# Performance work log

Hardware: AMD Instinct MI355X
Metric: run time of the kernel (lower is better)

The kernel has to match this reference:

```python
import jax, jax.numpy as jnp
import numpy as np

# ---- Cl(3,0) Cayley table derivation (pure Python, done once at import) ----
_BASIS_GENS = [(), (1,), (2,), (3,), (1, 2), (1, 3), (2, 3), (1, 2, 3)]
_GENS_TO_IDX = {g: i for i, g in enumerate(_BASIS_GENS)}

def _reduce_product(a_gens, b_gens):
    gens = list(a_gens) + list(b_gens)
    sign = 1
    changed = True
    while changed:
        changed = False
        i = 0
        while i < len(gens) - 1:
            if gens[i] == gens[i + 1]:
                gens.pop(i); gens.pop(i)
                changed = True
                if i > 0:
                    i -= 1
            elif gens[i] > gens[i + 1]:
                gens[i], gens[i + 1] = gens[i + 1], gens[i]
                sign *= -1
                changed = True
                i += 1
            else:
                i += 1
    return _GENS_TO_IDX[tuple(gens)], sign

def _k_groups():
    gi = [[] for _ in range(8)]
    gj = [[] for _ in range(8)]
    gs = [[] for _ in range(8)]
    for i in range(8):
        for j in range(8):
            k, s = _reduce_product(_BASIS_GENS[i], _BASIS_GENS[j])
            gi[k].append(i); gj[k].append(j); gs[k].append(float(s))
    return np.array(gi), np.array(gj), np.array(gs, dtype=np.float32)

KG_I, KG_J, KG_S = _k_groups()  # each (8, 8): for target blade k, 8 (i,j,sign) contributions
LN_EPS = 1e-5


def setup_inputs() -> dict:
    key = jax.random.key(0)
    ks = jax.random.split(key, 6)
    B, T, N, D, Fdim = 4, 4096, 8, 128, 512
    return {
        "x": jax.random.normal(ks[0], (B, T, N, D), dtype=jnp.float32),
        "interaction_weights": 0.1 * jax.random.normal(ks[1], (N, N), dtype=jnp.float32),
        "w_gate": 0.02 * jax.random.normal(ks[2], (D, Fdim), dtype=jnp.float32),
        "w_up": 0.02 * jax.random.normal(ks[3], (D, Fdim), dtype=jnp.float32),
        "w_down": 0.02 * jax.random.normal(ks[4], (Fdim, D), dtype=jnp.float32),
        "ln_gamma": jnp.ones((D,), dtype=jnp.float32),
        "ln_beta": jnp.zeros((D,), dtype=jnp.float32),
        "geo_gate": jnp.float32(0.5),
    }


def reference(x, interaction_weights, w_gate, w_up, w_down, ln_gamma, ln_beta, geo_gate):
    # x: (B, T, 8, D)
    kg_i = jnp.asarray(KG_I)
    kg_j = jnp.asarray(KG_J)
    kg_s = jnp.asarray(KG_S)

    # K-grouped Cayley geometric self-product
    w = jax.nn.sigmoid(interaction_weights)          # (8, 8)
    sw = kg_s * w[kg_i, kg_j]                        # (8, 8): sign * weight per (k, pair)
    x_i = x[:, :, kg_i, :]                           # (B, T, 8, 8, D)
    x_j = x[:, :, kg_j, :]                           # (B, T, 8, 8, D)
    geo = jnp.sum(x_i * x_j * sw[None, None, :, :, None], axis=3)  # (B, T, 8, D)

    # gate-mix geo with residual stream
    gate = jax.nn.sigmoid(geo_gate)
    mixed = gate * geo + (1.0 - gate) * x

    # LayerNorm over last dim
    mu = jnp.mean(mixed, axis=-1, keepdims=True)
    var = jnp.var(mixed, axis=-1, keepdims=True)
    normed = (mixed - mu) / jnp.sqrt(var + LN_EPS) * ln_gamma + ln_beta

    # per-blade SwiGLU FFN
    g = normed @ w_gate                              # (B, T, 8, F)
    u = normed @ w_up
    out = (jax.nn.silu(g) * u) @ w_down              # (B, T, 8, D)
    return x + out
```

## Files before the change

### kernel.cpp

```cpp
#include <hip/hip_runtime.h>


typedef __bf16 bf16x8 __attribute__((ext_vector_type(8)));
typedef float  f32x4  __attribute__((ext_vector_type(4)));

#define MFMA16(a, b, c) __builtin_amdgcn_mfma_f32_16x16x32_bf16((a), (b), (c), 0, 0, 0)

constexpr int OFF_WG = 0;
constexpr int OFF_WU = 131072;
constexpr int OFF_WD = 262144;
constexpr int OFF_C  = 393216;

__device__ __forceinline__ float fexp2(float x) {
  float r; asm("v_exp_f32 %0, %1" : "=v"(r) : "v"(x)); return r;
}
__device__ __forceinline__ float frcp(float x) {
  float r; asm("v_rcp_f32 %0, %1" : "=v"(r) : "v"(x)); return r;
}
__device__ __forceinline__ float fsigmoid(float x) {
  return frcp(1.f + fexp2(-1.44269504088896f * x));
}
__device__ __forceinline__ unsigned cvtbf(float f) {
  unsigned u = __builtin_bit_cast(unsigned, f);
  return (u + 0x7fffu + ((u >> 16) & 1u)) >> 16;
}
__device__ __forceinline__ unsigned pack2(float a, float b) {
  return cvtbf(a) | (cvtbf(b) << 16);
}

__device__ constexpr int PIdx[7][4][2] = {
  {{0,1},{2,4},{3,5},{6,7}},
  {{0,2},{1,4},{3,6},{5,7}},
  {{0,3},{1,5},{2,6},{4,7}},
  {{0,4},{1,2},{3,7},{5,6}},
  {{0,5},{1,3},{2,7},{4,6}},
  {{0,6},{1,7},{2,3},{4,5}},
  {{0,7},{1,6},{2,5},{3,4}}};

__global__ __launch_bounds__(256) void k_prep(
    const float* __restrict__ W, const float* __restrict__ wg,
    const float* __restrict__ wu, const float* __restrict__ wd,
    const float* __restrict__ gg, char* __restrict__ ws) {
  int gid = blockIdx.x * 256 + threadIdx.x;
  if (gid < 65536) {
    int f = gid & 511, k = gid >> 9;
    unsigned short v = (unsigned short)cvtbf(wg[k * 512 + f]);
    int fl = f & 63;
    int off = OFF_WG + (f >> 6) * 16384 + ((fl * 256 + k * 2) ^ ((f & 7) << 4));
    *(unsigned short*)(ws + off) = v;
  } else if (gid < 131072) {
    int t = gid - 65536;
    int f = t & 511, k = t >> 9;
    unsigned short v = (unsigned short)cvtbf(wu[k * 512 + f]);
    int fl = f & 63;
    int off = OFF_WU + (f >> 6) * 16384 + ((fl * 256 + k * 2) ^ ((f & 7) << 4));
    *(unsigned short*)(ws + off) = v;
  } else {
    int t = gid - 131072;
    int d = t & 127, f = t >> 7;
    unsigned short v = (unsigned short)cvtbf(wd[f * 128 + d]);
    int fl = f & 63;
    int off = OFF_WD + (f >> 6) * 16384 + ((d * 128 + fl * 2) ^ ((d & 7) << 4));
    *(unsigned short*)(ws + off) = v;
  }
  if (blockIdx.x == 0 && threadIdx.x == 0) {
    float s[64];
    for (int i = 0; i < 64; ++i) s[i] = fsigmoid(W[i]);
    float* C = (float*)(ws + OFF_C);
#define Sij(i, j) s[(i) * 8 + (j)]
    for (int i = 0; i < 8; ++i) C[i] = (i < 4 ? 1.f : -1.f) * Sij(i, i);
    C[8]  =  Sij(0,1) + Sij(1,0);  C[9]  = -Sij(2,4) + Sij(4,2);
    C[10] = -Sij(3,5) + Sij(5,3);  C[11] = -Sij(6,7) - Sij(7,6);
    C[12] =  Sij(0,2) + Sij(2,0);  C[13] =  Sij(1,4) - Sij(4,1);
    C[14] = -Sij(3,6) + Sij(6,3);  C[15] =  Sij(5,7) + Sij(7,5);
    C[16] =  Sij(0,3) + Sij(3,0);  C[17] =  Sij(1,5) - Sij(5,1);
    C[18] =  Sij(2,6) - Sij(6,2);  C[19] = -Sij(4,7) - Sij(7,4);
    C[20] =  Sij(0,4) + Sij(4,0);  C[21] =  Sij(1,2) - Sij(2,1);
    C[22] =  Sij(3,7) + Sij(7,3);  C[23] = -Sij(5,6) + Sij(6,5);
    C[24] =  Sij(0,5) + Sij(5,0);  C[25] =  Sij(1,3) - Sij(3,1);
    C[26] = -Sij(2,7) - Sij(7,2);  C[27] =  Sij(4,6) - Sij(6,4);
    C[28] =  Sij(0,6) + Sij(6,0);  C[29] =  Sij(1,7) + Sij(7,1);
    C[30] =  Sij(2,3) - Sij(3,2);  C[31] = -Sij(4,5) + Sij(5,4);
    C[32] =  Sij(0,7) + Sij(7,0);  C[33] =  Sij(1,6) + Sij(6,1);
    C[34] = -Sij(2,5) - Sij(5,2);  C[35] =  Sij(3,4) + Sij(4,3);
#undef Sij
    float gate = fsigmoid(gg[0]);
    C[36] = gate; C[37] = 1.f - gate;
  }
}

__global__ __launch_bounds__(256, 2) void k_fused(
    const float* __restrict__ x,
    const float* __restrict__ gamma,
    const float* __restrict__ beta,
    const float* __restrict__ cws,
    float* __restrict__ out,
    const char* __restrict__ ws) {
  __shared__ __align__(16) char lds[81920];
  const int tid = threadIdx.x, l = tid & 63, w = tid >> 6;
  const int r16 = l & 15, g4 = l >> 4;
  const long wrow0 = (long)blockIdx.x * 256 + (long)w * 64;

  char* scr = lds + 49152 + w * 8192;

#define STAGE(fcv)                                                             \
  _Pragma("unroll") for (int j = 0; j < 12; ++j) {                             \
    int o = (w * 12 + j) * 1024 + l * 16;                                      \
    const char* src = ws + (o >> 14) * 131072 + (fcv) * 16384 + (o & 16383);   \
    __builtin_amdgcn_global_load_lds(                                          \
        (const __attribute__((address_space(1))) unsigned*)src,                \
        (__attribute__((address_space(3))) unsigned*)(lds + (w * 12 + j) * 1024), \
        16, 0, 0);                                                             \
  }

  STAGE(0);

  float C[38];
#pragma unroll
  for (int i = 0; i < 38; ++i) C[i] = cws[i];
  const float gate = C[36], omg = C[37];

  bf16x8 bn[4][4];
#pragma unroll
  for (int p = 0; p < 4; ++p) {
#pragma unroll
    for (int hB = 0; hB < 2; ++hB) {
      const long r0 = wrow0 + p * 16 + hB * 8;
      float xa[8], xb[8];
#pragma unroll
      for (int n = 0; n < 8; ++n) {
        float2 v = *(const float2*)(x + (size_t)(r0 + n) * 128 + 2 * l);
        xa[n] = v.x; xb[n] = v.y;
      }
      float ga[8], gb[8];
      {
        float a0 = C[0] * xa[0] * xa[0], b0 = C[0] * xb[0] * xb[0];
#pragma unroll
        for (int i = 1; i < 8; ++i) {
          a0 = fmaf(C[i], xa[i] * xa[i], a0);
          b0 = fmaf(C[i], xb[i] * xb[i], b0);
        }
        ga[0] = a0; gb[0] = b0;
#pragma unroll
        for (int k = 1; k < 8; ++k) {
          float ta = 0.f, tb = 0.f;
#pragma unroll
          for (int q = 0; q < 4; ++q) {
            const int i = PIdx[k - 1][q][0], jj = PIdx[k - 1][q][1];
            const float c = C[8 + (k - 1) * 4 + q];
            ta = fmaf(c, xa[i] * xa[jj], ta);
            tb = fmaf(c, xb[i] * xb[jj], tb);
          }
          ga[k] = ta; gb[k] = tb;
        }
      }
#pragma unroll
      for (int n = 0; n < 8; ++n) {
        float2 m2;
        m2.x = fmaf(gate, ga[n], omg * xa[n]);
        m2.y = fmaf(gate, gb[n], omg * xb[n]);
        const int sr = hB * 8 + n;
        *(float2*)(scr + sr * 512 + ((l * 8) ^ (n << 4))) = m2;
      }
    }
    f32x4 mx[4][2];
    float s = 0.f, ss = 0.f;
    const int swr = (r16 & 7) << 4;
#pragma unroll
    for (int ks = 0; ks < 4; ++ks)
#pragma unroll
      for (int hh = 0; hh < 2; ++hh) {
        f32x4 v = *(const f32x4*)(scr + r16 * 512 +
                                  ((ks * 128 + g4 * 32 + hh * 16) ^ swr));
        mx[ks][hh] = v;
#pragma unroll
        for (int e = 0; e < 4; ++e) { s += v[e]; ss = fmaf(v[e], v[e], ss); }
      }
    s  += __shfl_xor(s, 16);  s  += __shfl_xor(s, 32);
    ss += __shfl_xor(ss, 16); ss += __shfl_xor(ss, 32);
    const float mean = s * (1.f / 128.f);
    const float var  = fmaf(-mean, mean, ss * (1.f / 128.f));
    const float rstd = rsqrtf(var + 1e-5f);
#pragma unroll
    for (int ks = 0; ks < 4; ++ks) {
      const float4 gm0 = *(const float4*)(gamma + ks * 32 + g4 * 8);
      const float4 gm1 = *(const float4*)(gamma + ks * 32 + g4 * 8 + 4);
      const float4 be0 = *(const float4*)(beta + ks * 32 + g4 * 8);
      const float4 be1 = *(const float4*)(beta + ks * 32 + g4 * 8 + 4);
      float nv[8];
      nv[0] = fmaf((mx[ks][0][0] - mean) * rstd, gm0.x, be0.x);
      nv[1] = fmaf((mx[ks][0][1] - mean) * rstd, gm0.y, be0.y);
      nv[2] = fmaf((mx[ks][0][2] - mean) * rstd, gm0.z, be0.z);
      nv[3] = fmaf((mx[ks][0][3] - mean) * rstd, gm0.w, be0.w);
      nv[4] = fmaf((mx[ks][1][0] - mean) * rstd, gm1.x, be1.x);
      nv[5] = fmaf((mx[ks][1][1] - mean) * rstd, gm1.y, be1.y);
      nv[6] = fmaf((mx[ks][1][2] - mean) * rstd, gm1.z, be1.z);
      nv[7] = fmaf((mx[ks][1][3] - mean) * rstd, gm1.w, be1.w);
      uint4 uv;
      uv.x = pack2(nv[0], nv[1]); uv.y = pack2(nv[2], nv[3]);
      uv.z = pack2(nv[4], nv[5]); uv.w = pack2(nv[6], nv[7]);
      bn[p][ks] = __builtin_bit_cast(bf16x8, uv);
    }
  }

  __syncthreads();

  f32x4 acc[8][4];
#pragma unroll
  for (int dt = 0; dt < 8; ++dt)
#pragma unroll
    for (int rt = 0; rt < 4; ++rt) acc[dt][rt] = f32x4{0.f, 0.f, 0.f, 0.f};

  const char* lwg = lds;
  const char* lwu = lds + 16384;
  const char* lwd = lds + 32768;
  char* lht = scr;

  for (int fc = 0; fc < 8; ++fc) {
#pragma unroll
    for (int ft = 0; ft < 4; ++ft) {
      const int fl = ft * 16 + r16, swzf = (fl & 7) << 4;
      bf16x8 ag[4], au[4];
#pragma unroll
      for (int ks = 0; ks < 4; ++ks) {
        const int kb = ks * 64 + g4 * 16;
        ag[ks] = *(const bf16x8*)(lwg + fl * 256 + (kb ^ swzf));
        au[ks] = *(const bf16x8*)(lwu + fl * 256 + (kb ^ swzf));
      }
#pragma unroll
      for (int rt = 0; rt < 4; ++rt) {
        f32x4 cg = {0.f, 0.f, 0.f, 0.f}, cu = {0.f, 0.f, 0.f, 0.f};
#pragma unroll
        for (int ks = 0; ks < 4; ++ks) {
          cg = MFMA16(ag[ks], bn[rt][ks], cg);
          cu = MFMA16(au[ks], bn[rt][ks], cu);
        }
        const float h0 = cg[0] * cu[0] * frcp(1.f + fexp2(-1.44269504f * cg[0]));
        const float h1 = cg[1] * cu[1] * frcp(1.f + fexp2(-1.44269504f * cg[1]));
        const float h2 = cg[2] * cu[2] * frcp(1.f + fexp2(-1.44269504f * cg[2]));
        const float h3 = cg[3] * cu[3] * frcp(1.f + fexp2(-1.44269504f * cg[3]));
        uint2 hv; hv.x = pack2(h0, h1); hv.y = pack2(h2, h3);
        const int row = rt * 16 + r16;
        *(uint2*)(lht + row * 128 + ((ft * 32 + g4 * 8) ^ ((row & 7) << 4))) = hv;
      }
    }
    bf16x8 hb[4][2];
#pragma unroll
    for (int rt = 0; rt < 4; ++rt)
#pragma unroll
      for (int k2 = 0; k2 < 2; ++k2) {
        const int row = rt * 16 + r16;
        hb[rt][k2] = *(const bf16x8*)(lht + row * 128 +
                                      ((k2 * 64 + g4 * 16) ^ ((row & 7) << 4)));
      }
#pragma unroll
    for (int dt = 0; dt < 8; ++dt) {
      const int d = dt * 16 + r16, swzd = (d & 7) << 4;
      bf16x8 w0 = *(const bf16x8*)(lwd + d * 128 + ((g4 * 16) ^ swzd));
      bf16x8 w1 = *(const bf16x8*)(lwd + d * 128 + ((64 + g4 * 16) ^ swzd));
#pragma unroll
      for (int rt = 0; rt < 4; ++rt) {
        acc[dt][rt] = MFMA16(w0, hb[rt][0], acc[dt][rt]);
        acc[dt][rt] = MFMA16(w1, hb[rt][1], acc[dt][rt]);
      }
    }
    if (fc < 7) {
      __syncthreads();
      STAGE(fc + 1);
      __syncthreads();
    }
  }
#undef STAGE

#pragma unroll
  for (int dt = 0; dt < 8; ++dt)
#pragma unroll
    for (int rt = 0; rt < 4; ++rt) {
      const size_t row = (size_t)(wrow0 + rt * 16 + r16);
      const int db = dt * 16 + g4 * 4;
      const float4 xv = *(const float4*)(x + row * 128 + db);
      float4 o;
      o.x = acc[dt][rt][0] + xv.x;
      o.y = acc[dt][rt][1] + xv.y;
      o.z = acc[dt][rt][2] + xv.z;
      o.w = acc[dt][rt][3] + xv.w;
      *(float4*)(out + row * 128 + db) = o;
    }
}


extern "C" void kernel_launch(void* const* d_in, const int* in_sizes, int n_in,
                              void* d_out, int out_size, void* d_ws, size_t ws_size,
                              hipStream_t stream) {
  (void)in_sizes; (void)n_in; (void)out_size; (void)ws_size;
  const float* x     = (const float*)d_in[0];
  const float* W     = (const float*)d_in[1];
  const float* wg    = (const float*)d_in[2];
  const float* wu    = (const float*)d_in[3];
  const float* wd    = (const float*)d_in[4];
  const float* gamma = (const float*)d_in[5];
  const float* beta  = (const float*)d_in[6];
  const float* gg    = (const float*)d_in[7];
  char* ws = (char*)d_ws;

  k_prep<<<768, 256, 0, stream>>>(W, wg, wu, wd, gg, ws);
  k_fused<<<512, 256, 0, stream>>>(x, gamma, beta, (const float*)(ws + OFF_C),
                                   (float*)d_out, ws);
}
```

Baseline: 205.5 us.

## Read FFN weights directly from global memory instead of staging through LDS

Repacks the bf16 gate/up/down weights in the prep kernel into a fragment-major layout, so each lane's 16-byte MFMA operand sits contiguously and a wavefront's loads coalesce. The fused kernel then loads these fragments straight from global memory (L2/cache) and drops the LDS staging and the block-wide barriers around each chunk. LDS shrinks to the per-wave activation scratch, which could allow more blocks per CU. The cost is more global/L2 traffic per wave and exposed load latency ahead of the MFMAs, with no explicit prefetch.

```diff
diff --git a/kernel.cpp b/kernel.cpp
--- a/kernel.cpp
+++ b/kernel.cpp
@@ -45,22 +45,22 @@
   if (gid < 65536) {
     int f = gid & 511, k = gid >> 9;
     unsigned short v = (unsigned short)cvtbf(wg[k * 512 + f]);
-    int fl = f & 63;
-    int off = OFF_WG + (f >> 6) * 16384 + ((fl * 256 + k * 2) ^ ((f & 7) << 4));
+    int off = OFF_WG + (f >> 6) * 16384 + (k >> 5) * 4096 +
+              ((k >> 3) & 3) * 1024 + (f & 63) * 16 + (k & 7) * 2;
     *(unsigned short*)(ws + off) = v;
   } else if (gid < 131072) {
     int t = gid - 65536;
     int f = t & 511, k = t >> 9;
     unsigned short v = (unsigned short)cvtbf(wu[k * 512 + f]);
-    int fl = f & 63;
-    int off = OFF_WU + (f >> 6) * 16384 + ((fl * 256 + k * 2) ^ ((f & 7) << 4));
+    int off = OFF_WU + (f >> 6) * 16384 + (k >> 5) * 4096 +
+              ((k >> 3) & 3) * 1024 + (f & 63) * 16 + (k & 7) * 2;
     *(unsigned short*)(ws + off) = v;
   } else {
     int t = gid - 131072;
     int d = t & 127, f = t >> 7;
     unsigned short v = (unsigned short)cvtbf(wd[f * 128 + d]);
-    int fl = f & 63;
-    int off = OFF_WD + (f >> 6) * 16384 + ((d * 128 + fl * 2) ^ ((d & 7) << 4));
+    int off = OFF_WD + (f >> 6) * 16384 + ((f >> 5) & 1) * 8192 +
+              ((f >> 3) & 3) * 2048 + d * 16 + (f & 7) * 2;
     *(unsigned short*)(ws + off) = v;
   }
   if (blockIdx.x == 0 && threadIdx.x == 0) {
@@ -96,24 +96,12 @@
     const float* __restrict__ cws,
     float* __restrict__ out,
     const char* __restrict__ ws) {
-  __shared__ __align__(16) char lds[81920];
+  __shared__ __align__(16) char lds[32768];
   const int tid = threadIdx.x, l = tid & 63, w = tid >> 6;
   const int r16 = l & 15, g4 = l >> 4;
   const long wrow0 = (long)blockIdx.x * 256 + (long)w * 64;
 
-  char* scr = lds + 49152 + w * 8192;
-
-#define STAGE(fcv)                                                             \
-  _Pragma("unroll") for (int j = 0; j < 12; ++j) {                             \
-    int o = (w * 12 + j) * 1024 + l * 16;                                      \
-    const char* src = ws + (o >> 14) * 131072 + (fcv) * 16384 + (o & 16383);   \
-    __builtin_amdgcn_global_load_lds(                                          \
-        (const __attribute__((address_space(1))) unsigned*)src,                \
-        (__attribute__((address_space(3))) unsigned*)(lds + (w * 12 + j) * 1024), \
-        16, 0, 0);                                                             \
-  }
-
-  STAGE(0);
+  char* scr = lds + w * 8192;
 
   float C[38];
 #pragma unroll
@@ -203,29 +191,27 @@
     }
   }
 
-  __syncthreads();
-
   f32x4 acc[8][4];
 #pragma unroll
   for (int dt = 0; dt < 8; ++dt)
 #pragma unroll
     for (int rt = 0; rt < 4; ++rt) acc[dt][rt] = f32x4{0.f, 0.f, 0.f, 0.f};
 
-  const char* lwg = lds;
-  const char* lwu = lds + 16384;
-  const char* lwd = lds + 32768;
   char* lht = scr;
+  const char* wsg = ws + OFF_WG + g4 * 1024;
+  const char* wsu = ws + OFF_WU + g4 * 1024;
+  const char* wsd = ws + OFF_WD + g4 * 2048;
 
   for (int fc = 0; fc < 8; ++fc) {
+    const int cb = fc * 16384;
 #pragma unroll
     for (int ft = 0; ft < 4; ++ft) {
-      const int fl = ft * 16 + r16, swzf = (fl & 7) << 4;
+      const int fo = (ft * 16 + r16) * 16;
       bf16x8 ag[4], au[4];
 #pragma unroll
       for (int ks = 0; ks < 4; ++ks) {
-        const int kb = ks * 64 + g4 * 16;
-        ag[ks] = *(const bf16x8*)(lwg + fl * 256 + (kb ^ swzf));
-        au[ks] = *(const bf16x8*)(lwu + fl * 256 + (kb ^ swzf));
+        ag[ks] = *(const bf16x8*)(wsg + cb + ks * 4096 + fo);
+        au[ks] = *(const bf16x8*)(wsu + cb + ks * 4096 + fo);
       }
 #pragma unroll
       for (int rt = 0; rt < 4; ++rt) {
@@ -255,22 +241,16 @@
       }
 #pragma unroll
     for (int dt = 0; dt < 8; ++dt) {
-      const int d = dt * 16 + r16, swzd = (d & 7) << 4;
-      bf16x8 w0 = *(const bf16x8*)(lwd + d * 128 + ((g4 * 16) ^ swzd));
-      bf16x8 w1 = *(const bf16x8*)(lwd + d * 128 + ((64 + g4 * 16) ^ swzd));
+      const int dofs = (dt * 16 + r16) * 16;
+      bf16x8 w0 = *(const bf16x8*)(wsd + cb + dofs);
+      bf16x8 w1 = *(const bf16x8*)(wsd + cb + 8192 + dofs);
 #pragma unroll
       for (int rt = 0; rt < 4; ++rt) {
         acc[dt][rt] = MFMA16(w0, hb[rt][0], acc[dt][rt]);
         acc[dt][rt] = MFMA16(w1, hb[rt][1], acc[dt][rt]);
       }
     }
-    if (fc < 7) {
-      __syncthreads();
-      STAGE(fc + 1);
-      __syncthreads();
-    }
-  }
-#undef STAGE
+  }
 
 #pragma unroll
   for (int dt = 0; dt < 8; ++dt)
```

Result: no change. 202.0 us (-1.7%).
